# Optimization experiments

Hardware: AMD Instinct MI355X
Metric: run time of the kernel (lower is better)

Reference implementation:

```python
import jax, jax.numpy as jnp
import numpy as np

B, S, E, H = 1, 2048, 1024, 16
D = E // H  # head_dim = 64
MAX_POS = 2048
NEG_INF = -1e30


def _rotary(x):
    # x: [B, S, H, D]; positions along axis 1
    half = D // 2
    inv_freq = 1.0 / (10000.0 ** (jnp.arange(0, D, 2, dtype=jnp.float32) / D))  # [D/2]
    freqs = jnp.arange(S, dtype=jnp.float32)[:, None] * inv_freq[None, :]       # [S, D/2]
    emb = jnp.concatenate([freqs, freqs], axis=-1)                              # [S, D]
    cos = jnp.cos(emb)[None, :, None, :]
    sin = jnp.sin(emb)[None, :, None, :]
    x1, x2 = x[..., :half], x[..., half:]
    rot = jnp.concatenate([-x2, x1], axis=-1)
    return x * cos + rot * sin


def setup_inputs() -> dict:
    key = jax.random.key(0)
    ks = jax.random.split(key, 8)
    w = lambda k: (jax.random.normal(k, (E, E), jnp.float32) * 0.02)
    inp = {
        "x": jax.random.normal(ks[0], (B, S, E), jnp.float32),
        "mask": jnp.tril(jnp.ones((S, S), jnp.int32)),  # causal 0/1 mask
        "Wq": w(ks[1]), "bq": jnp.zeros((E,), jnp.float32),
        "Wk": w(ks[2]), "bk": jnp.zeros((E,), jnp.float32),
        "Wv": w(ks[3]), "bv": jnp.zeros((E,), jnp.float32),
        "Wo": w(ks[4]), "bo": jnp.zeros((E,), jnp.float32),
        "rel_pos_emb": jax.random.normal(ks[5], (2 * MAX_POS - 1, D), jnp.float32) * 0.02,
    }
    return inp


def reference(x, mask, Wq, bq, Wk, bk, Wv, bv, Wo, bo, rel_pos_emb):
    scale = D ** -0.5
    q = (x @ Wq + bq).reshape(B, S, H, D)
    k = (x @ Wk + bk).reshape(B, S, H, D)
    v = (x @ Wv + bv).reshape(B, S, H, D)
    q = _rotary(q)
    k = _rotary(k)
    # [B, H, S, D]
    qh = jnp.swapaxes(q, 1, 2)
    kh = jnp.swapaxes(k, 1, 2)
    vh = jnp.swapaxes(v, 1, 2)
    scores = jnp.einsum('bhid,bhjd->bhij', qh, kh) * scale  # [B,H,S,S]
    # relative position bias (Shaw-style: gather then contract with q)
    pos = jnp.arange(S)
    bucket = pos[None, :] - pos[:, None] + S - 1            # [S,S] in [0, 2S-2]
    rel = rel_pos_emb[bucket]                               # [S,S,D]
    scores = scores + jnp.einsum('bhid,ijd->bhij', qh, rel)
    scores = jnp.where(mask[None, None, :, :] == 0, NEG_INF, scores)
    attn = jax.nn.softmax(scores, axis=-1)
    out = jnp.einsum('bhij,bhjd->bhid', attn, vh)           # [B,H,S,D]
    out = jnp.swapaxes(out, 1, 2).reshape(B, S, E)
    return out @ Wo + bo
```

## Files before the change

kernel.cpp:

```cpp
#include <hip/hip_runtime.h>
#include <hip/hip_bf16.h>

typedef __attribute__((ext_vector_type(8))) short bf16x8;
typedef __attribute__((ext_vector_type(4))) float f32x4;

#define MFMA16(a,b,c) __builtin_amdgcn_mfma_f32_16x16x32_bf16((a),(b),(c),0,0,0)
#define GLDS16(g, l) __builtin_amdgcn_global_load_lds((const __attribute__((address_space(1))) void*)(g), (__attribute__((address_space(3))) void*)(l), 16, 0, 0)

static constexpr int S_ = 2048, E_ = 1024, H_ = 16;
static constexpr float QS = 0.125f * 1.44269504f;

__device__ __forceinline__ unsigned pk2(float a, float b) {
  __hip_bfloat16 ba = __float2bfloat16(a), bb = __float2bfloat16(b);
  return (unsigned)*(unsigned short*)&ba | ((unsigned)*(unsigned short*)&bb << 16);
}
__device__ __forceinline__ float ubf(unsigned short u) {
  return __uint_as_float((unsigned)u << 16);
}

__global__ __launch_bounds__(256) void prep_k(const float* __restrict__ x, const float* __restrict__ rel,
                                              const float* __restrict__ Wq, const float* __restrict__ Wk,
                                              const float* __restrict__ Wv, const float* __restrict__ Wo,
                                              const float* __restrict__ bq, const float* __restrict__ bk,
                                              const float* __restrict__ bv,
                                              __hip_bfloat16* __restrict__ xb, __hip_bfloat16* __restrict__ relb,
                                              __hip_bfloat16* __restrict__ wqkvT, __hip_bfloat16* __restrict__ woT,
                                              float* __restrict__ bqkv, float* __restrict__ cost,
                                              float* __restrict__ sint) {
  int blk = blockIdx.x, tid = threadIdx.x;
  if (blk < 1024) {
    __shared__ float tile[64][65];
    int wsel = blk >> 8, sub = blk & 255;
    const float* W = wsel == 0 ? Wq : wsel == 1 ? Wk : wsel == 2 ? Wv : Wo;
    __hip_bfloat16* WT = wsel < 3 ? wqkvT + (size_t)wsel * E_ * E_ : woT;
    int bx = sub & 15, by = sub >> 4;
    for (int i = tid; i < 4096; i += 256) {
      int ki = i >> 6, ni = i & 63;
      tile[ki][ni] = W[(size_t)(by*64 + ki) * E_ + bx*64 + ni];
    }
    __syncthreads();
    for (int i = tid; i < 4096; i += 256) {
      int ni = i >> 6, ki = i & 63;
      WT[(size_t)(bx*64 + ni) * E_ + by*64 + ki] = __float2bfloat16(tile[ki][ni]);
    }
  } else if (blk < 3072) {
    int i = (blk - 1024) * 256 + tid;
    float4 v = reinterpret_cast<const float4*>(x)[i];
    xb[4*i+0] = __float2bfloat16(v.x);
    xb[4*i+1] = __float2bfloat16(v.y);
    xb[4*i+2] = __float2bfloat16(v.z);
    xb[4*i+3] = __float2bfloat16(v.w);
  } else if (blk < 3328) {
    int i = (blk - 3072) * 256 + tid;
    if (i < 65520) {
      float4 v = reinterpret_cast<const float4*>(rel)[i];
      relb[4*i+0] = __float2bfloat16(v.x * 8.f);
      relb[4*i+1] = __float2bfloat16(v.y * 8.f);
      relb[4*i+2] = __float2bfloat16(v.z * 8.f);
      relb[4*i+3] = __float2bfloat16(v.w * 8.f);
    }
  } else if (blk < 3584) {
    int idx = (blk - 3328) * 256 + tid;
    int f = idx & 31, s = idx >> 5;
    float inv = powf(10000.f, -(float)f * (1.f/32.f));
    float a = (float)s * inv;
    cost[idx] = cosf(a);
    sint[idx] = sinf(a);
  } else {
    int i = (blk - 3584) * 256 + tid;
    if (i < 3072) bqkv[i] = i < 1024 ? bq[i] : (i < 2048 ? bk[i-1024] : bv[i-2048]);
  }
}

template<int BM, int MODE>
__global__ __launch_bounds__(256) void gemm_k(const __hip_bfloat16* __restrict__ A,
                                              const __hip_bfloat16* __restrict__ BT,
                                              const float* __restrict__ bias,
                                              const float* __restrict__ cost,
                                              const float* __restrict__ sint,
                                              __hip_bfloat16* __restrict__ qhh,
                                              __hip_bfloat16* __restrict__ khh,
                                              __hip_bfloat16* __restrict__ vb,
                                              float* __restrict__ outf,
                                              int K) {
  constexpr int MI = BM/32;
  __shared__ __hip_bfloat16 As[2][BM*64];
  __shared__ __hip_bfloat16 Bs[2][128*64];
  int tid = threadIdx.x, lane = tid & 63, w = tid >> 6;
  int rowq = lane & 15, hi = lane >> 4, ksel = hi << 3;
  int wr = (w >> 1) * (BM/2), wc = (w & 1) * 64;
  int m0 = blockIdx.y * BM, n0 = blockIdx.x * 128;
  int l3 = lane >> 3, l7 = lane & 7;
  f32x4 acc[MI][4] = {};

  auto stage = [&](int k0, int buf) {
    const char* Ap = (const char*)A + ((size_t)(m0 + w*(BM/4)) * K + k0) * 2;
    const char* Bp = (const char*)BT + ((size_t)(n0 + w*32) * K + k0) * 2;
    char* Ad = (char*)&As[buf][w*(BM/4)*64];
    char* Bd = (char*)&Bs[buf][w*32*64];
    for (int i = 0; i < MI; ++i)
      GLDS16(Ap + (size_t)(i*8 + l3)*(K*2) + l7*16, Ad + i*1024);
    for (int i = 0; i < 4; ++i)
      GLDS16(Bp + (size_t)(i*8 + l3)*(K*2) + l7*16, Bd + i*1024);
  };

  stage(0, 0);
  __syncthreads();
  int buf = 0;
  int nk = K >> 6;
  for (int t = 0; t < nk; ++t) {
    if (t + 1 < nk) stage((t+1)*64, buf^1);
    for (int kk = 0; kk < 64; kk += 32) {
      bf16x8 a[MI], b[4];
      for (int i = 0; i < MI; ++i) a[i] = *(const bf16x8*)&As[buf][(wr + i*16 + rowq)*64 + kk + ksel];
      for (int j = 0; j < 4; ++j)  b[j] = *(const bf16x8*)&Bs[buf][(wc + j*16 + rowq)*64 + kk + ksel];
      for (int i = 0; i < MI; ++i)
        for (int j = 0; j < 4; ++j)
          acc[i][j] = MFMA16(a[i], b[j], acc[i][j]);
    }
    __syncthreads();
    buf ^= 1;
  }

  if constexpr (MODE == 0) {
    int matsel = n0 >> 10, ncol = n0 & 1023;
    float bcol[4];
    for (int j = 0; j < 4; ++j) bcol[j] = bias[n0 + wc + j*16 + rowq];
    if (matsel < 2) {
      __hip_bfloat16* dst = matsel ? khh : qhh;
      float qs = matsel ? 1.0f : QS;
      for (int i = 0; i < MI; ++i)
        for (int rg = 0; rg < 4; ++rg) {
          int s = m0 + wr + i*16 + hi*4 + rg;
          for (int j = 0; j < 2; ++j) {
            int colp = ncol + wc + j*16 + rowq;
            int hh = colp >> 6, f = colp & 31;
            float c = cost[s*32 + f], sn = sint[s*32 + f];
            float v1 = acc[i][j][rg]   + bcol[j];
            float v2 = acc[i][j+2][rg] + bcol[j+2];
            dst[((size_t)hh*S_ + s)*64 + f]      = __float2bfloat16((v1*c - v2*sn) * qs);
            dst[((size_t)hh*S_ + s)*64 + f + 32] = __float2bfloat16((v2*c + v1*sn) * qs);
          }
        }
    } else {
      for (int i = 0; i < MI; ++i)
        for (int rg = 0; rg < 4; ++rg) {
          int s = m0 + wr + i*16 + hi*4 + rg;
          for (int j = 0; j < 4; ++j)
            vb[(size_t)s*E_ + ncol + wc + j*16 + rowq] = __float2bfloat16(acc[i][j][rg] + bcol[j]);
        }
    }
  } else {
    for (int i = 0; i < MI; ++i)
      for (int rg = 0; rg < 4; ++rg) {
        int row = m0 + wr + i*16 + hi*4 + rg;
        for (int j = 0; j < 4; ++j) {
          int col = n0 + wc + j*16 + rowq;
          outf[(size_t)row*E_ + col] = acc[i][j][rg] + bias[col];
        }
      }
  }
}

__global__ __launch_bounds__(256) void vtrans_k(const __hip_bfloat16* __restrict__ vb,
                                                __hip_bfloat16* __restrict__ vt) {
  __shared__ __hip_bfloat16 tile[64][72];
  int sb = blockIdx.x, h = blockIdx.y, tid = threadIdx.x;
  int r = tid >> 3, c = (tid & 7) * 8;
  *(int4*)&tile[r][c]    = *(const int4*)(vb + (size_t)(sb*64 + r)*E_ + h*64 + c);
  *(int4*)&tile[r+32][c] = *(const int4*)(vb + (size_t)(sb*64 + r+32)*E_ + h*64 + c);
  __syncthreads();
  int d = tid >> 3, s0 = (tid & 7) * 8;
  __hip_bfloat16 bufa[8], bufb[8];
  for (int j = 0; j < 8; ++j) bufa[j] = tile[s0+j][d];
  for (int j = 0; j < 8; ++j) bufb[j] = tile[s0+j][d+32];
  *(int4*)(vt + ((size_t)h*64 + d)*S_ + sb*64 + s0)    = *(int4*)bufa;
  *(int4*)(vt + ((size_t)h*64 + d+32)*S_ + sb*64 + s0) = *(int4*)bufb;
}

__global__ __launch_bounds__(256,2) void attn_k(const __hip_bfloat16* __restrict__ qh,
                                                const __hip_bfloat16* __restrict__ kh,
                                                const __hip_bfloat16* __restrict__ vt,
                                                const __hip_bfloat16* __restrict__ relb,
                                                __hip_bfloat16* __restrict__ opart,
                                                float2* __restrict__ ml) {
  int h = blockIdx.x & 15, p = blockIdx.x >> 4;
  int tid = threadIdx.x, lane = tid & 63, w = tid >> 6;
  int rowq = lane & 15, hi = lane >> 4, ksel = hi << 3;
  int l3 = lane >> 3, l7 = lane & 7;
  int swz = (l7*16) ^ (l3 << 4);
  __shared__ __hip_bfloat16 Ks[2][4096];
  __shared__ __hip_bfloat16 Vs[2][4096];
  __shared__ char WPb[4][4096];
  char* wp = WPb[w] + rowq*256;
  int sw8 = (rowq & 7) << 4;
  int pcol0 = ((hi*16)      ^ ((rowq & 7) << 4)) >> 1;
  int pcol1 = ((64 + hi*16) ^ ((rowq & 7) << 4)) >> 1;

  for (int ph = 0; ph < 2; ++ph) {
    int qb = ph ? 31 - p : p;
    int T = qb + 1;
    int t0 = ph ? (T + 1) >> 1 : 0;
    int t1 = ph ? T : (T + 1) >> 1;
    int i0w = qb*64 + w*16;

    const __hip_bfloat16* qrow = qh + ((size_t)h*S_ + i0w + rowq)*64 + ksel;
    bf16x8 q0 = *(const bf16x8*)(qrow);
    bf16x8 q1 = *(const bf16x8*)(qrow + 32);
    f32x4 o[4] = {};
    float m = -1e30f, l = 0.f;

    auto stage = [&](int t, int buf) {
      int j0 = t * 64;
      const char* kp = (const char*)(kh + ((size_t)h*S_ + j0 + w*16)*64);
      const char* vp = (const char*)(vt + ((size_t)(h*64 + w*16))*S_ + j0);
      char* kd = (char*)&Ks[buf][w*16*64];
      char* vd = (char*)&Vs[buf][w*16*64];
      for (int i = 0; i < 2; ++i) {
        GLDS16(kp + (size_t)(i*8 + l3)*128  + swz, kd + i*1024);
        GLDS16(vp + (size_t)(i*8 + l3)*4096 + swz, vd + i*1024);
      }
    };
    auto ldrel = [&](int t, bf16x8* r) {
      const __hip_bfloat16* rp = relb + (size_t)(t*64 - i0w + 2032 + rowq)*64 + ksel;
      #pragma unroll
      for (int nf = 0; nf < 5; ++nf) {
        r[nf*2]   = *(const bf16x8*)(rp + nf*1024);
        r[nf*2+1] = *(const bf16x8*)(rp + nf*1024 + 32);
      }
    };

    if (t0 < t1) {
      bf16x8 rc[10], rn[10];
      ldrel(t0, rc);
      stage(t0, 0);
      __syncthreads();
      int buf = 0;
      for (int t = t0; t < t1; ++t) {
        bool more = (t + 1 < t1);
        if (more) { stage(t+1, buf^1); ldrel(t+1, rn); }

        f32x4 sa[4] = {};
        f32x4 wt[5] = {};
        __builtin_amdgcn_s_setprio(1);
        for (int kk = 0; kk < 2; ++kk) {
          bf16x8 qf = kk ? q1 : q0;
          int pc = kk ? pcol1 : pcol0;
          for (int nf = 0; nf < 4; ++nf) {
            bf16x8 kf = *(const bf16x8*)&Ks[buf][(nf*16 + rowq)*64 + pc];
            sa[nf] = MFMA16(kf, qf, sa[nf]);
          }
          for (int nf = 0; nf < 5; ++nf)
            wt[nf] = MFMA16(rc[nf*2+kk], qf, wt[nf]);
        }
        __builtin_amdgcn_s_setprio(0);

        #pragma unroll
        for (int nf = 0; nf < 5; ++nf) {
          uint2 u = { pk2(wt[nf][0], wt[nf][1]), pk2(wt[nf][2], wt[nf][3]) };
          *(uint2*)(wp + ((nf*32 + hi*8) ^ sw8)) = u;
        }

        float sv[4][4];
        float tm = -1e30f;
        bool diag = (t == qb);
        #pragma unroll
        for (int nf = 0; nf < 4; ++nf)
          #pragma unroll
          for (int rg = 0; rg < 4; ++rg) {
            int kl = nf*16 + hi*4 + rg;
            float v = sa[nf][rg] + ubf(*(const unsigned short*)(wp + ((2*kl + 30 - 2*rowq) ^ sw8)));
            if (diag && kl > w*16 + rowq) v = -1e30f;
            sv[nf][rg] = v;
            tm = fmaxf(tm, v);
          }
        tm = fmaxf(tm, __shfl_xor(tm, 16));
        tm = fmaxf(tm, __shfl_xor(tm, 32));
        float mnew = fmaxf(m, tm);
        float al = exp2f(m - mnew);
        m = mnew;
        float ls = 0.f;
        float pe[4][4];
        #pragma unroll
        for (int nf = 0; nf < 4; ++nf)
          #pragma unroll
          for (int rg = 0; rg < 4; ++rg) {
            float e = exp2f(sv[nf][rg] - mnew);
            pe[nf][rg] = e;
            ls += e;
          }
        l = l * al + ls;
        #pragma unroll
        for (int nf = 0; nf < 4; ++nf) {
          uint2 u = { pk2(pe[nf][0], pe[nf][1]), pk2(pe[nf][2], pe[nf][3]) };
          *(uint2*)(wp + ((nf*32 + hi*8) ^ sw8)) = u;
        }
        float alq[4];
        #pragma unroll
        for (int rg = 0; rg < 4; ++rg) alq[rg] = __shfl(al, hi*4 + rg, 16);
        #pragma unroll
        for (int df = 0; df < 4; ++df)
          #pragma unroll
          for (int rg = 0; rg < 4; ++rg) o[df][rg] *= alq[rg];

        __builtin_amdgcn_s_setprio(1);
        for (int kk = 0; kk < 2; ++kk) {
          bf16x8 a = *(const bf16x8*)(wp + ((kk*64 + hi*16) ^ sw8));
          int pc = kk ? pcol1 : pcol0;
          for (int df = 0; df < 4; ++df) {
            bf16x8 b = *(const bf16x8*)&Vs[buf][(df*16 + rowq)*64 + pc];
            o[df] = MFMA16(a, b, o[df]);
          }
        }
        __builtin_amdgcn_s_setprio(0);
        __syncthreads();
        buf ^= 1;
        if (more) {
          #pragma unroll
          for (int i = 0; i < 10; ++i) rc[i] = rn[i];
        }
      }
    }

    float lt = l;
    lt += __shfl_xor(lt, 16);
    lt += __shfl_xor(lt, 32);
    if (lane < 16) ml[((size_t)ph*S_ + i0w + rowq)*H_ + h] = make_float2(m, lt);
    #pragma unroll
    for (int df = 0; df < 4; ++df)
      #pragma unroll
      for (int rg = 0; rg < 4; ++rg)
        opart[(size_t)ph*S_*E_ + (size_t)(i0w + hi*4 + rg)*E_ + h*64 + df*16 + rowq] =
            __float2bfloat16(o[df][rg]);
    __syncthreads();
  }
}

__global__ __launch_bounds__(256) void combine_k(const __hip_bfloat16* __restrict__ opart,
                                                 const float2* __restrict__ ml,
                                                 __hip_bfloat16* __restrict__ aout) {
  int r = blockIdx.x, tid = threadIdx.x;
  int c = tid * 4, h = c >> 6;
  float2 a0 = ml[(size_t)r*H_ + h];
  float2 a1 = ml[((size_t)S_ + r)*H_ + h];
  float M = fmaxf(a0.x, a1.x);
  float w0 = exp2f(a0.x - M), w1 = exp2f(a1.x - M);
  float dinv = 1.0f / (w0*a0.y + w1*a1.y);
  w0 *= dinv; w1 *= dinv;
  const unsigned short* o0 = (const unsigned short*)opart + (size_t)r*E_ + c;
  const unsigned short* o1 = o0 + (size_t)S_*E_;
  ushort4 u0 = *(const ushort4*)o0;
  ushort4 u1 = *(const ushort4*)o1;
  __hip_bfloat16 res[4];
  res[0] = __float2bfloat16(w0*ubf(u0.x) + w1*ubf(u1.x));
  res[1] = __float2bfloat16(w0*ubf(u0.y) + w1*ubf(u1.y));
  res[2] = __float2bfloat16(w0*ubf(u0.z) + w1*ubf(u1.z));
  res[3] = __float2bfloat16(w0*ubf(u0.w) + w1*ubf(u1.w));
  *(ushort4*)((unsigned short*)aout + (size_t)r*E_ + c) = *(ushort4*)res;
}

extern "C" void kernel_launch(void* const* d_in, const int* in_sizes, int n_in,
                              void* d_out, int out_size, void* d_ws, size_t ws_size,
                              hipStream_t stream) {
  const float* x   = (const float*)d_in[0];
  const float* Wq  = (const float*)d_in[2];
  const float* bq  = (const float*)d_in[3];
  const float* Wk  = (const float*)d_in[4];
  const float* bk  = (const float*)d_in[5];
  const float* Wv  = (const float*)d_in[6];
  const float* bv  = (const float*)d_in[7];
  const float* Wo  = (const float*)d_in[8];
  const float* bo  = (const float*)d_in[9];
  const float* rel = (const float*)d_in[10];
  float* out = (float*)d_out;

  char* ws = (char*)d_ws;
  size_t off = 0;
  auto alloc = [&](size_t bytes) -> void* {
    void* p = ws + off;
    off = (off + bytes + 255) & ~(size_t)255;
    return p;
  };
  __hip_bfloat16* xb    = (__hip_bfloat16*)alloc((size_t)S_*E_*2);
  __hip_bfloat16* wqkvT = (__hip_bfloat16*)alloc((size_t)3*E_*E_*2);
  __hip_bfloat16* vbuf  = (__hip_bfloat16*)alloc((size_t)S_*E_*2);
  float* cost = (float*)alloc((size_t)S_*32*4);
  float* sint = (float*)alloc((size_t)S_*32*4);
  float* bqkv = (float*)alloc((size_t)3072*4);
  if (off < (size_t)16*1024*1024) off = (size_t)16*1024*1024;
  __hip_bfloat16* woT   = (__hip_bfloat16*)alloc((size_t)E_*E_*2);
  __hip_bfloat16* relb  = (__hip_bfloat16*)alloc((size_t)4095*64*2);
  __hip_bfloat16* qhh  = (__hip_bfloat16*)alloc((size_t)S_*E_*2);
  __hip_bfloat16* khh  = (__hip_bfloat16*)alloc((size_t)S_*E_*2);
  __hip_bfloat16* vth  = (__hip_bfloat16*)alloc((size_t)S_*E_*2);
  __hip_bfloat16* aout = (__hip_bfloat16*)alloc((size_t)S_*E_*2);
  float2* ml = (float2*)alloc((size_t)2*S_*H_*8);

  __hip_bfloat16* opart = (__hip_bfloat16*)ws;

  prep_k<<<3596, 256, 0, stream>>>(x, rel, Wq, Wk, Wv, Wo, bq, bk, bv,
                                   xb, relb, wqkvT, woT, bqkv, cost, sint);

  gemm_k<64,0><<<dim3(24,32), 256, 0, stream>>>(xb, wqkvT, bqkv, cost, sint,
                                                qhh, khh, vbuf, nullptr, E_);
  vtrans_k<<<dim3(S_/64, H_), 256, 0, stream>>>(vbuf, vth);

  attn_k<<<512, 256, 0, stream>>>(qhh, khh, vth, relb, opart, ml);
  combine_k<<<S_, 256, 0, stream>>>(opart, ml, aout);

  gemm_k<64,1><<<dim3(8,32), 256, 0, stream>>>(aout, woT, bo, nullptr, nullptr,
                                               nullptr, nullptr, nullptr, out, E_);
}
```

Measured before the change: 124.8 us.

## Fuse V transpose into QKV GEMM epilogue, defer softmax rescale, keep rel bias fp32

The QKV GEMM epilogue now writes V directly in head-transposed [H*D, S] layout with 4-element vector stores, removing the separate transpose kernel and its intermediate buffer. In attention, the relative-position bias tile is kept in fp32 shared memory instead of being packed to bf16, and P uses its own shared buffer. The next relative-bias prefetch now reuses the same registers after they are consumed, freeing about ten vector registers. The online-softmax rescale of the output accumulator is skipped whenever the new row max exceeds the running max by at most 8 in log2 units. This deferral trades fewer exp and multiply operations for a small risk of larger exponent values.

Result: faster. 114.4 us (-8.3%).

```diff
diff --git a/kernel.cpp b/kernel.cpp
--- a/kernel.cpp
+++ b/kernel.cpp
@@ -80,7 +80,7 @@
                                               const float* __restrict__ sint,
                                               __hip_bfloat16* __restrict__ qhh,
                                               __hip_bfloat16* __restrict__ khh,
-                                              __hip_bfloat16* __restrict__ vb,
+                                              __hip_bfloat16* __restrict__ vt,
                                               float* __restrict__ outf,
                                               int K) {
   constexpr int MI = BM/32;
@@ -144,10 +144,14 @@
         }
     } else {
       for (int i = 0; i < MI; ++i)
-        for (int rg = 0; rg < 4; ++rg) {
-          int s = m0 + wr + i*16 + hi*4 + rg;
-          for (int j = 0; j < 4; ++j)
-            vb[(size_t)s*E_ + ncol + wc + j*16 + rowq] = __float2bfloat16(acc[i][j][rg] + bcol[j]);
+        for (int j = 0; j < 4; ++j) {
+          int colp = ncol + wc + j*16 + rowq;
+          int hh = colp >> 6, d = colp & 63;
+          int s0b = m0 + wr + i*16 + hi*4;
+          __hip_bfloat16 tmp[4];
+          for (int rg = 0; rg < 4; ++rg)
+            tmp[rg] = __float2bfloat16(acc[i][j][rg] + bcol[j]);
+          *(ushort4*)(vt + ((size_t)hh*64 + d)*S_ + s0b) = *(ushort4*)tmp;
         }
     }
   } else {
@@ -160,22 +164,6 @@
         }
       }
   }
-}
-
-__global__ __launch_bounds__(256) void vtrans_k(const __hip_bfloat16* __restrict__ vb,
-                                                __hip_bfloat16* __restrict__ vt) {
-  __shared__ __hip_bfloat16 tile[64][72];
-  int sb = blockIdx.x, h = blockIdx.y, tid = threadIdx.x;
-  int r = tid >> 3, c = (tid & 7) * 8;
-  *(int4*)&tile[r][c]    = *(const int4*)(vb + (size_t)(sb*64 + r)*E_ + h*64 + c);
-  *(int4*)&tile[r+32][c] = *(const int4*)(vb + (size_t)(sb*64 + r+32)*E_ + h*64 + c);
-  __syncthreads();
-  int d = tid >> 3, s0 = (tid & 7) * 8;
-  __hip_bfloat16 bufa[8], bufb[8];
-  for (int j = 0; j < 8; ++j) bufa[j] = tile[s0+j][d];
-  for (int j = 0; j < 8; ++j) bufb[j] = tile[s0+j][d+32];
-  *(int4*)(vt + ((size_t)h*64 + d)*S_ + sb*64 + s0)    = *(int4*)bufa;
-  *(int4*)(vt + ((size_t)h*64 + d+32)*S_ + sb*64 + s0) = *(int4*)bufb;
 }
 
 __global__ __launch_bounds__(256,2) void attn_k(const __hip_bfloat16* __restrict__ qh,
@@ -191,11 +179,14 @@
   int swz = (l7*16) ^ (l3 << 4);
   __shared__ __hip_bfloat16 Ks[2][4096];
   __shared__ __hip_bfloat16 Vs[2][4096];
-  __shared__ char WPb[4][4096];
-  char* wp = WPb[w] + rowq*256;
+  __shared__ float Wf[4][16*82];
+  __shared__ char  Psb[4][4096];
+  float* wrow = &Wf[w][rowq*82];
+  char* pp = Psb[w] + rowq*256;
   int sw8 = (rowq & 7) << 4;
   int pcol0 = ((hi*16)      ^ ((rowq & 7) << 4)) >> 1;
   int pcol1 = ((64 + hi*16) ^ ((rowq & 7) << 4)) >> 1;
+  int c0 = hi*4 + 15 - rowq;
 
   for (int ph = 0; ph < 2; ++ph) {
     int qb = ph ? 31 - p : p;
@@ -221,24 +212,24 @@
         GLDS16(vp + (size_t)(i*8 + l3)*4096 + swz, vd + i*1024);
       }
     };
-    auto ldrel = [&](int t, bf16x8* r) {
+    auto ldrel = [&](int t, bf16x8* rr) {
       const __hip_bfloat16* rp = relb + (size_t)(t*64 - i0w + 2032 + rowq)*64 + ksel;
       #pragma unroll
       for (int nf = 0; nf < 5; ++nf) {
-        r[nf*2]   = *(const bf16x8*)(rp + nf*1024);
-        r[nf*2+1] = *(const bf16x8*)(rp + nf*1024 + 32);
+        rr[nf*2]   = *(const bf16x8*)(rp + nf*1024);
+        rr[nf*2+1] = *(const bf16x8*)(rp + nf*1024 + 32);
       }
     };
 
     if (t0 < t1) {
-      bf16x8 rc[10], rn[10];
+      bf16x8 rc[10];
       ldrel(t0, rc);
       stage(t0, 0);
       __syncthreads();
       int buf = 0;
       for (int t = t0; t < t1; ++t) {
         bool more = (t + 1 < t1);
-        if (more) { stage(t+1, buf^1); ldrel(t+1, rn); }
+        if (more) stage(t+1, buf^1);
 
         f32x4 sa[4] = {};
         f32x4 wt[5] = {};
@@ -257,35 +248,48 @@
 
         #pragma unroll
         for (int nf = 0; nf < 5; ++nf) {
-          uint2 u = { pk2(wt[nf][0], wt[nf][1]), pk2(wt[nf][2], wt[nf][3]) };
-          *(uint2*)(wp + ((nf*32 + hi*8) ^ sw8)) = u;
-        }
+          *(float2*)(wrow + nf*16 + hi*4)     = make_float2(wt[nf][0], wt[nf][1]);
+          *(float2*)(wrow + nf*16 + hi*4 + 2) = make_float2(wt[nf][2], wt[nf][3]);
+        }
+
+        if (more) ldrel(t+1, rc);
 
         float sv[4][4];
+        #pragma unroll
+        for (int rg = 0; rg < 4; ++rg) {
+          int cc = c0 + rg;
+          #pragma unroll
+          for (int nf = 0; nf < 4; ++nf)
+            sv[nf][rg] = sa[nf][rg] + wrow[nf*16 + cc];
+        }
         float tm = -1e30f;
         bool diag = (t == qb);
+        int lim = w*16 + rowq;
         #pragma unroll
         for (int nf = 0; nf < 4; ++nf)
           #pragma unroll
           for (int rg = 0; rg < 4; ++rg) {
             int kl = nf*16 + hi*4 + rg;
-            float v = sa[nf][rg] + ubf(*(const unsigned short*)(wp + ((2*kl + 30 - 2*rowq) ^ sw8)));
-            if (diag && kl > w*16 + rowq) v = -1e30f;
-            sv[nf][rg] = v;
-            tm = fmaxf(tm, v);
+            if (diag && kl > lim) sv[nf][rg] = -1e30f;
+            tm = fmaxf(tm, sv[nf][rg]);
           }
         tm = fmaxf(tm, __shfl_xor(tm, 16));
         tm = fmaxf(tm, __shfl_xor(tm, 32));
-        float mnew = fmaxf(m, tm);
-        float al = exp2f(m - mnew);
-        m = mnew;
+
+        bool defer = __all(tm <= m + 8.0f);
+        float al = 1.0f;
+        if (!defer) {
+          float mnew = fmaxf(m, tm);
+          al = exp2f(m - mnew);
+          m = mnew;
+        }
         float ls = 0.f;
         float pe[4][4];
         #pragma unroll
         for (int nf = 0; nf < 4; ++nf)
           #pragma unroll
           for (int rg = 0; rg < 4; ++rg) {
-            float e = exp2f(sv[nf][rg] - mnew);
+            float e = exp2f(sv[nf][rg] - m);
             pe[nf][rg] = e;
             ls += e;
           }
@@ -293,19 +297,21 @@
         #pragma unroll
         for (int nf = 0; nf < 4; ++nf) {
           uint2 u = { pk2(pe[nf][0], pe[nf][1]), pk2(pe[nf][2], pe[nf][3]) };
-          *(uint2*)(wp + ((nf*32 + hi*8) ^ sw8)) = u;
-        }
-        float alq[4];
-        #pragma unroll
-        for (int rg = 0; rg < 4; ++rg) alq[rg] = __shfl(al, hi*4 + rg, 16);
-        #pragma unroll
-        for (int df = 0; df < 4; ++df)
+          *(uint2*)(pp + ((nf*32 + hi*8) ^ sw8)) = u;
+        }
+        if (!defer) {
+          float alq[4];
           #pragma unroll
-          for (int rg = 0; rg < 4; ++rg) o[df][rg] *= alq[rg];
+          for (int rg = 0; rg < 4; ++rg) alq[rg] = __shfl(al, hi*4 + rg, 16);
+          #pragma unroll
+          for (int df = 0; df < 4; ++df)
+            #pragma unroll
+            for (int rg = 0; rg < 4; ++rg) o[df][rg] *= alq[rg];
+        }
 
         __builtin_amdgcn_s_setprio(1);
         for (int kk = 0; kk < 2; ++kk) {
-          bf16x8 a = *(const bf16x8*)(wp + ((kk*64 + hi*16) ^ sw8));
+          bf16x8 a = *(const bf16x8*)(pp + ((kk*64 + hi*16) ^ sw8));
           int pc = kk ? pcol1 : pcol0;
           for (int df = 0; df < 4; ++df) {
             bf16x8 b = *(const bf16x8*)&Vs[buf][(df*16 + rowq)*64 + pc];
@@ -315,10 +321,6 @@
         __builtin_amdgcn_s_setprio(0);
         __syncthreads();
         buf ^= 1;
-        if (more) {
-          #pragma unroll
-          for (int i = 0; i < 10; ++i) rc[i] = rn[i];
-        }
       }
     }
 
@@ -383,7 +385,6 @@
   };
   __hip_bfloat16* xb    = (__hip_bfloat16*)alloc((size_t)S_*E_*2);
   __hip_bfloat16* wqkvT = (__hip_bfloat16*)alloc((size_t)3*E_*E_*2);
-  __hip_bfloat16* vbuf  = (__hip_bfloat16*)alloc((size_t)S_*E_*2);
   float* cost = (float*)alloc((size_t)S_*32*4);
   float* sint = (float*)alloc((size_t)S_*32*4);
   float* bqkv = (float*)alloc((size_t)3072*4);
@@ -402,8 +403,7 @@
                                    xb, relb, wqkvT, woT, bqkv, cost, sint);
 
   gemm_k<64,0><<<dim3(24,32), 256, 0, stream>>>(xb, wqkvT, bqkv, cost, sint,
-                                                qhh, khh, vbuf, nullptr, E_);
-  vtrans_k<<<dim3(S_/64, H_), 256, 0, stream>>>(vbuf, vth);
+                                                qhh, khh, vth, nullptr, E_);
 
   attn_k<<<512, 256, 0, stream>>>(qhh, khh, vth, relb, opart, ml);
   combine_k<<<S_, 256, 0, stream>>>(opart, ml, aout);
```
